# Kernel optimization log

Measured on AMD Instinct MI355X. Metric: run time of the kernel, lower is better.

Reference implementation:

```python
import jax, jax.numpy as jnp
import numpy as np

EPS = 1e-5  # InstanceNorm2d default


def setup_inputs() -> dict:
    key = jax.random.key(0)
    ks = jax.random.split(key, 8)
    B, L, D, Q, C, H, W = 16, 24, 256, 256, 256, 128, 128
    s = 0.05
    return {
        "w_source": jax.random.normal(ks[0], (B, L, D), jnp.float32),
        "w_target": jax.random.normal(ks[1], (B, L, D), jnp.float32),
        "h": jax.random.normal(ks[2], (B, C, H, W), jnp.float32),
        "conv0_w": jax.random.normal(ks[3], (Q, C), jnp.float32) * s,   # 1x1 conv kernel
        "conv0_b": jnp.zeros((Q,), jnp.float32),
        "fck_w": jax.random.normal(ks[4], (Q, D), jnp.float32) * s,
        "fck_b": jnp.zeros((Q,), jnp.float32),
        "fc_w": jax.random.normal(ks[5], (2 * C, D), jnp.float32) * s,
        "fc_b": jnp.zeros((2 * C,), jnp.float32),
        "in_w": jnp.ones((C,), jnp.float32),
        "in_b": jnp.zeros((C,), jnp.float32),
    }


def reference(w_source, w_target, h, conv0_w, conv0_b, fck_w, fck_b, fc_w, fc_b, in_w, in_b):
    # ---- CrossAttention ----
    # q: 1x1 conv over h  -> [B,H,W,Q]
    q = jnp.einsum("bchw,qc->bhwq", h, conv0_w) + conv0_b
    # k: word keys        -> [B,L,Q]
    k = jnp.einsum("bld,qd->blq", w_source, fck_w) + fck_b
    attn = jnp.einsum("bhwq,blq->bhwl", q, k)  # [B,H,W,L]

    # ---- MaskingAllocation ----
    scores = jnp.einsum("bld,bmd->blm", w_source, w_target)       # [B,L,L]
    left = jnp.sum(scores, axis=1, keepdims=True) - scores        # [B,L,L]
    idx = jnp.argmax(left, axis=-1)                               # [B,L]
    w_alloc = jnp.take_along_axis(w_target, idx[..., None], axis=1)  # [B,L,D]

    # ---- modulation params ----
    bg = jnp.einsum("bld,ed->ble", w_alloc, fc_w) + fc_b          # [B,L,2C]
    beta, gamma = jnp.split(bg, 2, axis=-1)                       # each [B,L,C]
    beta_map = jnp.einsum("bhwl,blc->bchw", attn, beta)           # [B,C,H,W]
    gamma_map = jnp.einsum("bhwl,blc->bchw", attn, gamma)

    # ---- InstanceNorm2d (affine) + modulation ----
    mean = jnp.mean(h, axis=(2, 3), keepdims=True)
    var = jnp.var(h, axis=(2, 3), keepdims=True)
    hn = (h - mean) * jax.lax.rsqrt(var + EPS)
    hn = hn * in_w[None, :, None, None] + in_b[None, :, None, None]
    return hn * gamma_map + beta_map
```

## Files before the change

kernel.cpp:

```cpp
#include <hip/hip_runtime.h>
#include <stdint.h>

#define HW 16384
#define Bn 16
#define Ln 24
#define Dn 256
#define Qn 256
#define Cn 256

typedef __attribute__((ext_vector_type(8))) short short8;
typedef __attribute__((ext_vector_type(4))) float f32x4;

__device__ __forceinline__ unsigned short f2bf(float f) {
  unsigned u = __builtin_bit_cast(unsigned, f);
  u += 0x7FFFu + ((u >> 16) & 1u);
  return (unsigned short)(u >> 16);
}
__device__ __forceinline__ float bf2f(unsigned short s) {
  return __builtin_bit_cast(float, (unsigned)s << 16);
}

__device__ __forceinline__ void gl_lds16(const void* gsrc, void* lds) {
  __builtin_amdgcn_global_load_lds(
      (const __attribute__((address_space(1))) unsigned int*)gsrc,
      (__attribute__((address_space(3))) unsigned int*)lds, 16, 0, 0);
}

__global__ void k_keys(const float* __restrict__ wsrc, const float* __restrict__ fckw,
                       const float* __restrict__ fckb, float* __restrict__ kmat) {
  int b = blockIdx.x / Ln, l = blockIdx.x % Ln;
  __shared__ float row[Dn];
  row[threadIdx.x] = wsrc[(b * Ln + l) * Dn + threadIdx.x];
  __syncthreads();
  int q = threadIdx.x;
  const float* wq = fckw + q * Dn;
  float acc = fckb[q];
#pragma unroll 8
  for (int d = 0; d < Dn; ++d) acc += row[d] * wq[d];
  kmat[(b * Ln + l) * Qn + q] = acc;
}

__global__ void k_alloc(const float* __restrict__ wsrc, const float* __restrict__ wtgt,
                        const float* __restrict__ conv0b, const float* __restrict__ kmat,
                        float* __restrict__ walloc, float* __restrict__ bias0) {
  int b = blockIdx.x;
  __shared__ float S[Ln][Dn];
  __shared__ float T[Ln][Dn];
  __shared__ double sc[Ln][Ln];
  __shared__ double cs[Ln];
  __shared__ int idx[Ln];
  int tid = threadIdx.x;
  for (int n = tid; n < Ln * Dn; n += 256) {
    S[n >> 8][n & 255] = wsrc[b * Ln * Dn + n];
    T[n >> 8][n & 255] = wtgt[b * Ln * Dn + n];
  }
  __syncthreads();
  for (int p = tid; p < Ln * Ln; p += 256) {
    int l = p / Ln, m = p % Ln;
    double a = 0.0;
    for (int d = 0; d < Dn; ++d) a += (double)S[l][d] * (double)T[m][d];
    sc[l][m] = a;
  }
  __syncthreads();
  if (tid < Ln) {
    double a = 0.0;
    for (int l = 0; l < Ln; ++l) a += sc[l][tid];
    cs[tid] = a;
  }
  __syncthreads();
  if (tid < Ln) {
    double best = -1e300; int bi = 0;
    for (int m = 0; m < Ln; ++m) {
      double v = cs[m] - sc[tid][m];
      if (v > best) { best = v; bi = m; }
    }
    idx[tid] = bi;
  }
  __syncthreads();
  for (int n = tid; n < Ln * Dn; n += 256) {
    int l = n >> 8, d = n & 255;
    walloc[b * Ln * Dn + n] = T[idx[l]][d];
  }
  if (tid < Ln) {
    float a = 0.f;
    const float* kr = kmat + (b * Ln + tid) * Qn;
    for (int q = 0; q < Qn; ++q) a += conv0b[q] * kr[q];
    bias0[b * Ln + tid] = a;
  }
}

__global__ void k_mbg(const float* __restrict__ kmat, const float* __restrict__ conv0w,
                      const float* __restrict__ walloc, const float* __restrict__ fcw,
                      const float* __restrict__ fcb,
                      float* __restrict__ Mmat, float* __restrict__ bg) {
  int bid = blockIdx.x;
  __shared__ float row[Dn];
  if (bid < Bn * Ln) {
    int b = bid / Ln, l = bid % Ln;
    row[threadIdx.x] = kmat[(b * Ln + l) * Qn + threadIdx.x];
    __syncthreads();
    int c = threadIdx.x;
    float acc = 0.f;
    for (int q = 0; q < Qn; ++q) acc += row[q] * conv0w[q * Cn + c];
    Mmat[(b * Ln + l) * Cn + c] = acc;
  } else {
    int id = bid - Bn * Ln;
    int b = id / Ln, l = id % Ln;
    row[threadIdx.x] = walloc[(b * Ln + l) * Dn + threadIdx.x];
    __syncthreads();
    for (int it = 0; it < 2; ++it) {
      int e = it * 256 + threadIdx.x;
      const float* we = fcw + e * Dn;
      float acc = fcb[e];
      for (int d = 0; d < Dn; ++d) acc += row[d] * we[d];
      bg[(b * Ln + l) * (2 * Cn) + e] = acc;
    }
  }
}

__global__ void k_gbuild(const float* __restrict__ Mmat, const float* __restrict__ bg,
                         const float* __restrict__ bias0,
                         unsigned short* __restrict__ Gt, float* __restrict__ bv) {
  int t = blockIdx.x, g = blockIdx.y, b = blockIdx.z;
  __shared__ float Ms[Ln][64];
  __shared__ float Gb[Ln][128];
  __shared__ float B0[Ln];
  __shared__ __align__(16) unsigned char img[16384];
  int tid = threadIdx.x;
  for (int n = tid; n < Ln * 64; n += 256) {
    int l = n >> 6, kk = n & 63;
    Ms[l][kk] = Mmat[(b * Ln + l) * Cn + t * 64 + kk];
  }
  for (int n = tid; n < Ln * 128; n += 256) {
    int l = n >> 7, j = n & 127;
    int half = j >> 6, r = j & 63;
    int e = (half == 0) ? (Cn + g * 64 + r) : (g * 64 + r);
    Gb[l][j] = bg[(b * Ln + l) * (2 * Cn) + e];
  }
  if (tid < Ln) B0[tid] = bias0[b * Ln + tid];
  __syncthreads();
  for (int i = 0; i < 32; ++i) {
    int n = i * 256 + tid;
    int m = n >> 6, kk = n & 63;
    float acc = 0.f;
#pragma unroll
    for (int l = 0; l < Ln; ++l) acc += Ms[l][kk] * Gb[l][m];
    unsigned off = (unsigned)((m * 128 + kk * 2) ^ ((m & 7) << 4));
    *(unsigned short*)(img + off) = f2bf(acc);
  }
  if (t == 0 && tid < 128) {
    float a = 0.f;
#pragma unroll
    for (int l = 0; l < Ln; ++l) a += B0[l] * Gb[l][tid];
    bv[b * 512 + g * 128 + tid] = a;
  }
  __syncthreads();
  unsigned long base = ((unsigned long)((b * 4 + g) * 4 + t)) * 16384ul;
  f32x4* dst = (f32x4*)((char*)Gt + base);
  const f32x4* srcv = (const f32x4*)img;
  for (int i = 0; i < 4; ++i) dst[i * 256 + tid] = srcv[i * 256 + tid];
}

__global__ void k_stats_tr(const float* __restrict__ h, unsigned short* __restrict__ hT,
                           float* __restrict__ part) {
  int hwc = blockIdx.x;
  int cc  = blockIdx.y;
  int b   = blockIdx.z;
  int tid = threadIdx.x;
  int w = tid >> 6, lane = tid & 63;
  __shared__ unsigned short tile[64 * 258];
  const int c0 = cc * 64, hw0 = hwc * 256;
  for (int i = 0; i < 16; ++i) {
    int cl = i * 4 + w;
    f32x4 v = *(const f32x4*)(h + ((unsigned long)(b * Cn + c0 + cl)) * HW + hw0 + lane * 4);
    float s  = v.x + v.y + v.z + v.w;
    float s2 = v.x * v.x + v.y * v.y + v.z * v.z + v.w * v.w;
#pragma unroll
    for (int o = 1; o < 64; o <<= 1) { s += __shfl_xor(s, o); s2 += __shfl_xor(s2, o); }
    if (lane == 0) {
      float* pp = part + (((unsigned long)(b * Cn + c0 + cl)) * 64 + hwc) * 2;
      pp[0] = s; pp[1] = s2;
    }
    unsigned lo = (unsigned)f2bf(v.x) | ((unsigned)f2bf(v.y) << 16);
    unsigned hi = (unsigned)f2bf(v.z) | ((unsigned)f2bf(v.w) << 16);
    unsigned* dst = (unsigned*)(tile + cl * 258 + lane * 4);
    dst[0] = lo; dst[1] = hi;
  }
  __syncthreads();
  for (int i = 0; i < 32; ++i) {
    int n = i * 256 + tid;
    int hw = n >> 5, cp = n & 31;
    unsigned short a0 = tile[(2 * cp) * 258 + hw];
    unsigned short a1 = tile[(2 * cp + 1) * 258 + hw];
    unsigned pk = (unsigned)a0 | ((unsigned)a1 << 16);
    *(unsigned*)(hT + ((unsigned long)b * HW + hw0 + hw) * Cn + c0 + 2 * cp) = pk;
  }
}

__global__ void k_fin(const float* __restrict__ part, const float* __restrict__ inw,
                      const float* __restrict__ inb, float* __restrict__ ss) {
  int id = blockIdx.x * 256 + threadIdx.x;
  int c = id & 255;
  float s = 0.f, s2 = 0.f;
  const float* pp = part + (unsigned long)id * 128;
  for (int j = 0; j < 64; ++j) { s += pp[2 * j]; s2 += pp[2 * j + 1]; }
  float mean = s * (1.0f / HW);
  float var = s2 * (1.0f / HW) - mean * mean;
  float rs = rsqrtf(var + 1e-5f);
  float scv = rs * inw[c];
  float sh = inb[c] - mean * scv;
  ss[id * 2] = scv; ss[id * 2 + 1] = sh;
}

__global__ __launch_bounds__(256, 2) void k_main(
    const unsigned short* __restrict__ hT, const unsigned short* __restrict__ Gt,
    const float* __restrict__ bv, const float* __restrict__ ss,
    float* __restrict__ out) {
  int hwt = blockIdx.x, g = blockIdx.y, b = blockIdx.z;
  int hw0 = hwt * 128;
  int tid = threadIdx.x;
  int w = tid >> 6, lane = tid & 63;
  int wr = w >> 1, wc = w & 1;
  int lr = lane & 15, lg = lane >> 4;

  __shared__ __align__(16) unsigned char Ab[2][16384];
  __shared__ __align__(16) unsigned char Bb[2][16384];

  const unsigned long blobBase = ((unsigned long)(b * 4 + g)) * 4ul * 16384ul;
  const unsigned short* hTb = hT + (unsigned long)b * HW * Cn;

  f32x4 acc[4][4];
#pragma unroll
  for (int i = 0; i < 4; ++i)
#pragma unroll
    for (int j = 0; j < 4; ++j) acc[i][j] = (f32x4){0.f, 0.f, 0.f, 0.f};

  unsigned short h16[2][4][4];

#pragma unroll
  for (int j = 0; j < 4; ++j) {
    int seg = j * 4 + w;
    unsigned a = seg * 1024 + lane * 16;
    gl_lds16((const char*)Gt + blobBase + a, &Ab[0][seg * 1024]);
    int hwR = a >> 7, blk = (a >> 4) & 7;
    const void* src = (const char*)(hTb + (unsigned long)(hw0 + hwR) * Cn) +
                      ((blk ^ (hwR & 7)) * 16);
    gl_lds16(src, &Bb[0][seg * 1024]);
  }

#pragma unroll
  for (int t = 0; t < 4; ++t) {
    __syncthreads();
    int cur = t & 1;
    if (t < 3) {
      int tn = t + 1, nb = tn & 1;
#pragma unroll
      for (int j = 0; j < 4; ++j) {
        int seg = j * 4 + w;
        unsigned a = seg * 1024 + lane * 16;
        gl_lds16((const char*)Gt + blobBase + (unsigned long)tn * 16384ul + a, &Ab[nb][seg * 1024]);
        int hwR = a >> 7, blk = (a >> 4) & 7;
        const void* src = (const char*)(hTb + (unsigned long)(hw0 + hwR) * Cn + tn * 64) +
                          ((blk ^ (hwR & 7)) * 16);
        gl_lds16(src, &Bb[nb][seg * 1024]);
      }
    }
    if (t == g) {
#pragma unroll
      for (int p = 0; p < 2; ++p)
#pragma unroll
        for (int jn = 0; jn < 4; ++jn)
#pragma unroll
          for (int r = 0; r < 4; ++r) {
            int ki = wr * 32 + p * 16 + lg * 4 + r;
            int row = wc * 64 + jn * 16 + lr;
            unsigned off = (unsigned)((row * 128 + ki * 2) ^ ((row & 7) << 4));
            h16[p][jn][r] = *(const unsigned short*)(&Bb[cur][0] + off);
          }
    }
#pragma unroll
    for (int kk = 0; kk < 2; ++kk) {
      short8 afr[4], bfr[4];
#pragma unroll
      for (int jm = 0; jm < 4; ++jm) {
        int row = (jm >> 1) * 64 + wr * 32 + (jm & 1) * 16 + lr;
        unsigned off = (unsigned)((row * 128 + kk * 64 + lg * 16) ^ ((row & 7) << 4));
        afr[jm] = *(const short8*)(&Ab[cur][0] + off);
      }
#pragma unroll
      for (int jn = 0; jn < 4; ++jn) {
        int row = wc * 64 + jn * 16 + lr;
        unsigned off = (unsigned)((row * 128 + kk * 64 + lg * 16) ^ ((row & 7) << 4));
        bfr[jn] = *(const short8*)(&Bb[cur][0] + off);
      }
#pragma unroll
      for (int jm = 0; jm < 4; ++jm)
#pragma unroll
        for (int jn = 0; jn < 4; ++jn)
          acc[jm][jn] = __builtin_amdgcn_mfma_f32_16x16x32_bf16(afr[jm], bfr[jn], acc[jm][jn], 0, 0, 0);
    }
  }

  const float* ssb = ss + (b * Cn) * 2;
  const float* bvb = bv + b * 512 + g * 128;
#pragma unroll
  for (int p = 0; p < 2; ++p) {
#pragma unroll
    for (int r = 0; r < 4; ++r) {
      int mloc = wr * 32 + p * 16 + lg * 4 + r;
      int cg = g * 64 + mloc;
      float scv = ssb[cg * 2], sh = ssb[cg * 2 + 1];
      float bvg = bvb[mloc];
      float bvbeta = bvb[64 + mloc];
#pragma unroll
      for (int jn = 0; jn < 4; ++jn) {
        float hv = bf2f(h16[p][jn][r]);
        float hn = hv * scv + sh;
        float gm = acc[p][jn][r] + bvg;
        float bt = acc[2 + p][jn][r] + bvbeta;
        int hwg = hw0 + wc * 64 + jn * 16 + lr;
        out[((unsigned long)(b * Cn + cg)) * HW + hwg] = hn * gm + bt;
      }
    }
  }
}

__global__ void k_sentinel(float* out) { out[0] = 12345.0f; }

extern "C" void kernel_launch(void* const* d_in, const int* in_sizes, int n_in,
                              void* d_out, int out_size, void* d_ws, size_t ws_size,
                              hipStream_t stream) {
  const float* wsrc   = (const float*)d_in[0];
  const float* wtgt   = (const float*)d_in[1];
  const float* h      = (const float*)d_in[2];
  const float* conv0w = (const float*)d_in[3];
  const float* conv0b = (const float*)d_in[4];
  const float* fckw   = (const float*)d_in[5];
  const float* fckb   = (const float*)d_in[6];
  const float* fcw    = (const float*)d_in[7];
  const float* fcb    = (const float*)d_in[8];
  const float* inw    = (const float*)d_in[9];
  const float* inb    = (const float*)d_in[10];
  float* out = (float*)d_out;
  char* ws = (char*)d_ws;

  const size_t NEED = 142542848ull;
  if (ws_size < NEED) {
    k_sentinel<<<1, 1, 0, stream>>>(out);
    return;
  }

  unsigned short* hT = (unsigned short*)(ws + 0);
  float* kmat   = (float*)(ws + 134217728);
  float* walloc = (float*)(ws + 134610944);
  float* bias0  = (float*)(ws + 135004160);
  float* bg     = (float*)(ws + 135006208);
  float* Mmat   = (float*)(ws + 135792640);
  unsigned short* Gt = (unsigned short*)(ws + 136185856);
  float* bv     = (float*)(ws + 140380160);
  float* part   = (float*)(ws + 140412928);
  float* ss     = (float*)(ws + 142510080);

  k_keys<<<Bn * Ln, 256, 0, stream>>>(wsrc, fckw, fckb, kmat);
  k_alloc<<<Bn, 256, 0, stream>>>(wsrc, wtgt, conv0b, kmat, walloc, bias0);
  k_mbg<<<2 * Bn * Ln, 256, 0, stream>>>(kmat, conv0w, walloc, fcw, fcb, Mmat, bg);
  dim3 gg(4, 4, Bn);
  k_gbuild<<<gg, 256, 0, stream>>>(Mmat, bg, bias0, Gt, bv);
  dim3 gs(64, 4, Bn);
  k_stats_tr<<<gs, 256, 0, stream>>>(h, hT, part);
  k_fin<<<16, 256, 0, stream>>>(part, inw, inb, ss);
  dim3 gm(128, 4, Bn);
  k_main<<<gm, 256, 0, stream>>>(hT, Gt, bv, ss, out);
}
```

Measured before the change: 335.2 us.

## Load GEMM operands directly from global memory and remap main-kernel blocks for L2 reuse

The main kernel no longer stages both GEMM operands through double-buffered LDS. It reads G and hT fragments straight from global memory into registers, and keeps only one LDS tile of h for the epilogue. The G matrix is now stored plain row-major instead of as pre-swizzled image tiles. Blocks are remapped over a 2D grid so the four channel groups sharing an hw tile run close together, which should improve L2 hits on hT. The stats reduction moves from per-row warp shuffles to an LDS reduction after the transpose, and the stats/transpose kernel now launches first. The risks are higher global-load latency without LDS pipelining, possible uncoalesced fragment reads, and stats computed from bf16-rounded values.

```diff
diff --git a/kernel.cpp b/kernel.cpp
--- a/kernel.cpp
+++ b/kernel.cpp
@@ -121,44 +121,32 @@
 __global__ void k_gbuild(const float* __restrict__ Mmat, const float* __restrict__ bg,
                          const float* __restrict__ bias0,
                          unsigned short* __restrict__ Gt, float* __restrict__ bv) {
-  int t = blockIdx.x, g = blockIdx.y, b = blockIdx.z;
-  __shared__ float Ms[Ln][64];
+  int g = blockIdx.x, b = blockIdx.y;
+  __shared__ float Ms[Ln][Dn];
   __shared__ float Gb[Ln][128];
   __shared__ float B0[Ln];
-  __shared__ __align__(16) unsigned char img[16384];
   int tid = threadIdx.x;
-  for (int n = tid; n < Ln * 64; n += 256) {
-    int l = n >> 6, kk = n & 63;
-    Ms[l][kk] = Mmat[(b * Ln + l) * Cn + t * 64 + kk];
-  }
+  for (int n = tid; n < Ln * Dn; n += 256) Ms[n >> 8][n & 255] = Mmat[b * Ln * Dn + n];
   for (int n = tid; n < Ln * 128; n += 256) {
     int l = n >> 7, j = n & 127;
-    int half = j >> 6, r = j & 63;
-    int e = (half == 0) ? (Cn + g * 64 + r) : (g * 64 + r);
+    int e = (j < 64) ? (Cn + g * 64 + j) : (g * 64 + (j - 64));
     Gb[l][j] = bg[(b * Ln + l) * (2 * Cn) + e];
   }
   if (tid < Ln) B0[tid] = bias0[b * Ln + tid];
   __syncthreads();
-  for (int i = 0; i < 32; ++i) {
-    int n = i * 256 + tid;
-    int m = n >> 6, kk = n & 63;
+  unsigned long base = (unsigned long)(b * 4 + g) * (128 * 256);
+  for (int m = 0; m < 128; ++m) {
     float acc = 0.f;
 #pragma unroll
-    for (int l = 0; l < Ln; ++l) acc += Ms[l][kk] * Gb[l][m];
-    unsigned off = (unsigned)((m * 128 + kk * 2) ^ ((m & 7) << 4));
-    *(unsigned short*)(img + off) = f2bf(acc);
-  }
-  if (t == 0 && tid < 128) {
+    for (int l = 0; l < Ln; ++l) acc += Ms[l][tid] * Gb[l][m];
+    Gt[base + (unsigned long)m * 256 + tid] = f2bf(acc);
+  }
+  if (tid < 128) {
     float a = 0.f;
 #pragma unroll
     for (int l = 0; l < Ln; ++l) a += B0[l] * Gb[l][tid];
     bv[b * 512 + g * 128 + tid] = a;
   }
-  __syncthreads();
-  unsigned long base = ((unsigned long)((b * 4 + g) * 4 + t)) * 16384ul;
-  f32x4* dst = (f32x4*)((char*)Gt + base);
-  const f32x4* srcv = (const f32x4*)img;
-  for (int i = 0; i < 4; ++i) dst[i * 256 + tid] = srcv[i * 256 + tid];
 }
 
 __global__ void k_stats_tr(const float* __restrict__ h, unsigned short* __restrict__ hT,
@@ -169,31 +157,39 @@
   int tid = threadIdx.x;
   int w = tid >> 6, lane = tid & 63;
   __shared__ unsigned short tile[64 * 258];
+  __shared__ float red[64 * 17 + 16];
   const int c0 = cc * 64, hw0 = hwc * 256;
   for (int i = 0; i < 16; ++i) {
     int cl = i * 4 + w;
     f32x4 v = *(const f32x4*)(h + ((unsigned long)(b * Cn + c0 + cl)) * HW + hw0 + lane * 4);
-    float s  = v.x + v.y + v.z + v.w;
-    float s2 = v.x * v.x + v.y * v.y + v.z * v.z + v.w * v.w;
-#pragma unroll
-    for (int o = 1; o < 64; o <<= 1) { s += __shfl_xor(s, o); s2 += __shfl_xor(s2, o); }
-    if (lane == 0) {
-      float* pp = part + (((unsigned long)(b * Cn + c0 + cl)) * 64 + hwc) * 2;
-      pp[0] = s; pp[1] = s2;
-    }
     unsigned lo = (unsigned)f2bf(v.x) | ((unsigned)f2bf(v.y) << 16);
     unsigned hi = (unsigned)f2bf(v.z) | ((unsigned)f2bf(v.w) << 16);
     unsigned* dst = (unsigned*)(tile + cl * 258 + lane * 4);
     dst[0] = lo; dst[1] = hi;
   }
   __syncthreads();
+  int cp = tid & 31, sub = tid >> 5;
+  float s0 = 0.f, s20 = 0.f, s1 = 0.f, s21 = 0.f;
   for (int i = 0; i < 32; ++i) {
-    int n = i * 256 + tid;
-    int hw = n >> 5, cp = n & 31;
+    int hw = i * 8 + sub;
     unsigned short a0 = tile[(2 * cp) * 258 + hw];
     unsigned short a1 = tile[(2 * cp + 1) * 258 + hw];
+    float f0 = bf2f(a0), f1 = bf2f(a1);
+    s0 += f0; s20 += f0 * f0; s1 += f1; s21 += f1 * f1;
     unsigned pk = (unsigned)a0 | ((unsigned)a1 << 16);
     *(unsigned*)(hT + ((unsigned long)b * HW + hw0 + hw) * Cn + c0 + 2 * cp) = pk;
+  }
+  red[(2 * cp) * 17 + sub * 2]     = s0;
+  red[(2 * cp) * 17 + sub * 2 + 1] = s20;
+  red[(2 * cp + 1) * 17 + sub * 2]     = s1;
+  red[(2 * cp + 1) * 17 + sub * 2 + 1] = s21;
+  __syncthreads();
+  if (tid < 64) {
+    float a = 0.f, q = 0.f;
+#pragma unroll
+    for (int j = 0; j < 8; ++j) { a += red[tid * 17 + j * 2]; q += red[tid * 17 + j * 2 + 1]; }
+    float* pp = part + (((unsigned long)(b * Cn + c0 + tid)) * 64 + hwc) * 2;
+    pp[0] = a; pp[1] = q;
   }
 }
 
@@ -216,90 +212,64 @@
     const unsigned short* __restrict__ hT, const unsigned short* __restrict__ Gt,
     const float* __restrict__ bv, const float* __restrict__ ss,
     float* __restrict__ out) {
-  int hwt = blockIdx.x, g = blockIdx.y, b = blockIdx.z;
+  int b = blockIdx.y;
+  unsigned x = blockIdx.x;
+  unsigned wg = (x & 7) * 64 + (x >> 3);
+  int g = wg & 3, hwt = wg >> 2;
   int hw0 = hwt * 128;
   int tid = threadIdx.x;
   int w = tid >> 6, lane = tid & 63;
   int wr = w >> 1, wc = w & 1;
   int lr = lane & 15, lg = lane >> 4;
 
-  __shared__ __align__(16) unsigned char Ab[2][16384];
-  __shared__ __align__(16) unsigned char Bb[2][16384];
-
-  const unsigned long blobBase = ((unsigned long)(b * 4 + g)) * 4ul * 16384ul;
+  __shared__ __align__(16) unsigned char Eb[16384];
+
+  const unsigned short* Gblob = Gt + (unsigned long)(b * 4 + g) * (128 * 256);
   const unsigned short* hTb = hT + (unsigned long)b * HW * Cn;
-
-  f32x4 acc[4][4];
-#pragma unroll
-  for (int i = 0; i < 4; ++i)
-#pragma unroll
-    for (int j = 0; j < 4; ++j) acc[i][j] = (f32x4){0.f, 0.f, 0.f, 0.f};
-
-  unsigned short h16[2][4][4];
 
 #pragma unroll
   for (int j = 0; j < 4; ++j) {
     int seg = j * 4 + w;
     unsigned a = seg * 1024 + lane * 16;
-    gl_lds16((const char*)Gt + blobBase + a, &Ab[0][seg * 1024]);
     int hwR = a >> 7, blk = (a >> 4) & 7;
-    const void* src = (const char*)(hTb + (unsigned long)(hw0 + hwR) * Cn) +
+    const void* src = (const char*)(hTb + (unsigned long)(hw0 + hwR) * Cn + g * 64) +
                       ((blk ^ (hwR & 7)) * 16);
-    gl_lds16(src, &Bb[0][seg * 1024]);
-  }
-
-#pragma unroll
-  for (int t = 0; t < 4; ++t) {
-    __syncthreads();
-    int cur = t & 1;
-    if (t < 3) {
-      int tn = t + 1, nb = tn & 1;
-#pragma unroll
-      for (int j = 0; j < 4; ++j) {
-        int seg = j * 4 + w;
-        unsigned a = seg * 1024 + lane * 16;
-        gl_lds16((const char*)Gt + blobBase + (unsigned long)tn * 16384ul + a, &Ab[nb][seg * 1024]);
-        int hwR = a >> 7, blk = (a >> 4) & 7;
-        const void* src = (const char*)(hTb + (unsigned long)(hw0 + hwR) * Cn + tn * 64) +
-                          ((blk ^ (hwR & 7)) * 16);
-        gl_lds16(src, &Bb[nb][seg * 1024]);
-      }
-    }
-    if (t == g) {
-#pragma unroll
-      for (int p = 0; p < 2; ++p)
-#pragma unroll
-        for (int jn = 0; jn < 4; ++jn)
-#pragma unroll
-          for (int r = 0; r < 4; ++r) {
-            int ki = wr * 32 + p * 16 + lg * 4 + r;
-            int row = wc * 64 + jn * 16 + lr;
-            unsigned off = (unsigned)((row * 128 + ki * 2) ^ ((row & 7) << 4));
-            h16[p][jn][r] = *(const unsigned short*)(&Bb[cur][0] + off);
-          }
-    }
-#pragma unroll
-    for (int kk = 0; kk < 2; ++kk) {
-      short8 afr[4], bfr[4];
-#pragma unroll
-      for (int jm = 0; jm < 4; ++jm) {
-        int row = (jm >> 1) * 64 + wr * 32 + (jm & 1) * 16 + lr;
-        unsigned off = (unsigned)((row * 128 + kk * 64 + lg * 16) ^ ((row & 7) << 4));
-        afr[jm] = *(const short8*)(&Ab[cur][0] + off);
-      }
-#pragma unroll
-      for (int jn = 0; jn < 4; ++jn) {
-        int row = wc * 64 + jn * 16 + lr;
-        unsigned off = (unsigned)((row * 128 + kk * 64 + lg * 16) ^ ((row & 7) << 4));
-        bfr[jn] = *(const short8*)(&Bb[cur][0] + off);
-      }
-#pragma unroll
-      for (int jm = 0; jm < 4; ++jm)
-#pragma unroll
-        for (int jn = 0; jn < 4; ++jn)
-          acc[jm][jn] = __builtin_amdgcn_mfma_f32_16x16x32_bf16(afr[jm], bfr[jn], acc[jm][jn], 0, 0, 0);
-    }
-  }
+    gl_lds16(src, &Eb[seg * 1024]);
+  }
+
+  f32x4 acc[4][4];
+#pragma unroll
+  for (int i = 0; i < 4; ++i)
+#pragma unroll
+    for (int j = 0; j < 4; ++j) acc[i][j] = (f32x4){0.f, 0.f, 0.f, 0.f};
+
+  const unsigned short* pA[4];
+  const unsigned short* pB[4];
+#pragma unroll
+  for (int jm = 0; jm < 4; ++jm) {
+    int rowA = (jm >> 1) * 64 + wr * 32 + (jm & 1) * 16 + lr;
+    pA[jm] = Gblob + rowA * 256 + lg * 8;
+  }
+#pragma unroll
+  for (int jn = 0; jn < 4; ++jn) {
+    pB[jn] = hTb + (unsigned long)(hw0 + wc * 64 + jn * 16 + lr) * Cn + lg * 8;
+  }
+
+#pragma unroll
+  for (int kk = 0; kk < 8; ++kk) {
+    short8 afr[4], bfr[4];
+#pragma unroll
+    for (int jm = 0; jm < 4; ++jm) afr[jm] = *(const short8*)(pA[jm] + kk * 32);
+#pragma unroll
+    for (int jn = 0; jn < 4; ++jn) bfr[jn] = *(const short8*)(pB[jn] + kk * 32);
+#pragma unroll
+    for (int jm = 0; jm < 4; ++jm)
+#pragma unroll
+      for (int jn = 0; jn < 4; ++jn)
+        acc[jm][jn] = __builtin_amdgcn_mfma_f32_16x16x32_bf16(afr[jm], bfr[jn], acc[jm][jn], 0, 0, 0);
+  }
+
+  __syncthreads();
 
   const float* ssb = ss + (b * Cn) * 2;
   const float* bvb = bv + b * 512 + g * 128;
@@ -314,7 +284,9 @@
       float bvbeta = bvb[64 + mloc];
 #pragma unroll
       for (int jn = 0; jn < 4; ++jn) {
-        float hv = bf2f(h16[p][jn][r]);
+        int row = wc * 64 + jn * 16 + lr;
+        unsigned off = (unsigned)((row * 128 + mloc * 2) ^ ((row & 7) << 4));
+        float hv = bf2f(*(const unsigned short*)(&Eb[0] + off));
         float hn = hv * scv + sh;
         float gm = acc[p][jn][r] + bvg;
         float bt = acc[2 + p][jn][r] + bvbeta;
@@ -361,14 +333,14 @@
   float* part   = (float*)(ws + 140412928);
   float* ss     = (float*)(ws + 142510080);
 
+  dim3 gs(64, 4, Bn);
+  k_stats_tr<<<gs, 256, 0, stream>>>(h, hT, part);
   k_keys<<<Bn * Ln, 256, 0, stream>>>(wsrc, fckw, fckb, kmat);
   k_alloc<<<Bn, 256, 0, stream>>>(wsrc, wtgt, conv0b, kmat, walloc, bias0);
   k_mbg<<<2 * Bn * Ln, 256, 0, stream>>>(kmat, conv0w, walloc, fcw, fcb, Mmat, bg);
-  dim3 gg(4, 4, Bn);
+  dim3 gg(4, Bn);
   k_gbuild<<<gg, 256, 0, stream>>>(Mmat, bg, bias0, Gt, bv);
-  dim3 gs(64, 4, Bn);
-  k_stats_tr<<<gs, 256, 0, stream>>>(h, hT, part);
   k_fin<<<16, 256, 0, stream>>>(part, inw, inb, ss);
-  dim3 gm(128, 4, Bn);
+  dim3 gm(512, Bn);
   k_main<<<gm, 256, 0, stream>>>(hT, Gt, bv, ss, out);
 }
```

Measured after the change: 458.5 us. +36.8%, slower.
